# Kernel tuning notes

Measured on AMD Instinct MI355X. Metric: run time of the kernel, lower is better.

Reference implementation:

```python
import jax, jax.numpy as jnp
import numpy as np

B, C, H, W = 32, 3, 512, 512
DOWNSAMPLE = 2
N = W // DOWNSAMPLE  # 256 glimpse points
SMALL = 1e-4


def setup_inputs() -> dict:
    key = jax.random.key(0)
    k1, k2 = jax.random.split(key)
    x = jax.random.normal(k1, (B, C, H, W), dtype=jnp.float32)
    # p = locnet output: (gx_raw, gy_raw, log_sigma2, log_delta, log_gamma)
    p = jax.random.normal(k2, (B, 5), dtype=jnp.float32) * 0.5
    return {"x": x, "p": p}


def _filterbank(g, sigma2, delta, size):
    # g, sigma2, delta: [B]; returns [B, N, size]
    i = jnp.arange(N, dtype=jnp.float32)
    a = jnp.arange(size, dtype=jnp.float32)
    mu = g[:, None] + delta[:, None] * (i - N / 2.0 - 0.5)          # [B, N]
    F = jnp.exp(-((a - mu[:, :, None]) ** 2) / 2.0 / sigma2[:, None, None])  # [B, N, size]
    return F / (F.sum(axis=-1, keepdims=True) + SMALL)


def reference(x, p):
    # attention params (matches _get_attention_params)
    gx = W * (p[:, 0] + 1.0) / 2.0
    gy = H * (p[:, 1] + 1.0) / 2.0
    sigma2 = jnp.exp(p[:, 2])
    delta = jnp.exp(p[:, 3]) * (max(W, H) - 1) / (N - 1.0)
    gamma = jnp.exp(p[:, 4])
    # Gaussian filterbanks
    Fx = _filterbank(gx, sigma2, delta, W)  # [B, N, W]
    Fy = _filterbank(gy, sigma2, delta, H)  # [B, N, H]
    # read: gamma * Fy @ x @ Fx^T, expressed as two batched GEMMs
    Fyx = jnp.einsum('bnh,bchw->bcnw', Fy, x)       # [B, C, N, W]
    out = jnp.einsum('bcnw,bmw->bcnm', Fyx, Fx)     # [B, C, N, N]
    return gamma[:, None, None, None] * out
```

## Files before the change

kernel.cpp:

```cpp
#include <hip/hip_runtime.h>
#include <hip/hip_bf16.h>
#include <math.h>


namespace {

typedef __attribute__((ext_vector_type(8))) short v8s;
typedef __attribute__((ext_vector_type(4))) short v4s;
typedef __attribute__((ext_vector_type(4))) float f32x4;

constexpr int Bn = 32;
constexpr int Cc = 3;
constexpr int HW = 512;
constexpr int Nn = 256;
constexpr float SMALLF = 1e-4f;

__device__ inline unsigned short f2bf(float f) {
    __hip_bfloat16 h = __float2bfloat16(f);
    union { __hip_bfloat16 h; unsigned short u; } c;
    c.h = h;
    return c.u;
}

__device__ inline int xcd_swz(int bid, int nwg) {
    return (bid & 7) * (nwg >> 3) + (bid >> 3);
}

__device__ inline bool tile_window_g(float g, float delta, float sigma,
                                     int r0, int Trows, int& klo, int& khi) {
    float lo = g + delta * ((float)r0 - 128.5f) - 4.5f * sigma - 2.0f;
    float hi = g + delta * ((float)(r0 + Trows - 1) - 128.5f) + 4.5f * sigma + 2.0f;
    if (hi < 0.0f || lo > 511.0f) return false;
    klo = max(0, (int)floorf(lo * (1.0f / 64.0f)));
    khi = min(7, (int)floorf(hi * (1.0f / 64.0f)));
    return khi >= klo;
}

__global__ __launch_bounds__(256) void fb_kernel(const float* __restrict__ p,
                                                 unsigned short* __restrict__ Fx,
                                                 unsigned short* __restrict__ Fy) {
    const int wid  = threadIdx.x >> 6;
    const int lane = threadIdx.x & 63;
    const int rid  = blockIdx.x * 4 + wid;
    const int which = rid >> 13;
    const int r = rid & 8191;
    const int b = r >> 8;
    const int n = r & 255;

    const float* pb = p + b * 5;
    const float sigma2 = expf(pb[2]);
    const float delta  = expf(pb[3]) * (511.0f / 255.0f);
    const float g = (which == 0) ? (HW * (pb[0] + 1.0f) * 0.5f)
                                 : (HW * (pb[1] + 1.0f) * 0.5f);
    const float mu = g + delta * ((float)n - 128.5f);
    const float inv2s = 0.5f / sigma2;

    float f[8];
    float sum = 0.0f;
#pragma unroll
    for (int q = 0; q < 8; ++q) {
        float a = (float)(q * 64 + lane);
        float d = a - mu;
        f[q] = expf(-d * d * inv2s);
        sum += f[q];
    }
#pragma unroll
    for (int s = 1; s < 64; s <<= 1) sum += __shfl_xor(sum, s, 64);
    const float inv = 1.0f / (sum + SMALLF);

    unsigned short* dst = ((which == 0) ? Fx : Fy) + ((size_t)(b * Nn + n)) * HW;
#pragma unroll
    for (int q = 0; q < 8; ++q) dst[q * 64 + lane] = f2bf(f[q] * inv);
}

__device__ inline v8s frag_read(const unsigned short* __restrict__ lds, int row, int kk, int lk) {
    int byte = row * 128 + (((kk * 64) + lk * 16) ^ ((row & 7) << 4));
    return *(const v8s*)((const char*)lds + byte);
}

__global__ __launch_bounds__(256) void gemm1_kernel(const float* __restrict__ x,
                                                    const unsigned short* __restrict__ Fx_b,
                                                    const float* __restrict__ p,
                                                    unsigned short* __restrict__ G) {
    __shared__ unsigned short lds_all[2 * 64 * 64];
    unsigned short* As = lds_all;
    unsigned short* Bs = lds_all + 64 * 64;
    const int t = threadIdx.x;
    const int wg = xcd_swz(blockIdx.x, 3072);
    const int bc = wg >> 5, b = bc / 3;
    const int rem = wg & 31;
    const int h0 = (rem >> 2) * 64;
    const int m0 = (rem & 3) * 64;

    const float* pb = p + b * 5;
    const float sigma = sqrtf(expf(pb[2]));
    const float delta = expf(pb[3]) * (511.0f / 255.0f);

    {
        const float gy = HW * (pb[1] + 1.0f) * 0.5f;
        int ulo, uhi;
        if (!tile_window_g(gy, delta, sigma, 0, 256, ulo, uhi)) return;
        int ht = h0 >> 6;
        if (ht < ulo || ht > uhi) return;
    }

    const float* Ag = x + (size_t)bc * HW * HW + (size_t)h0 * HW;
    const unsigned short* Bg = Fx_b + (size_t)b * Nn * HW + (size_t)m0 * HW;

    const float gx = HW * (pb[0] + 1.0f) * 0.5f;
    int klo = 0, khi = -1;
    bool live = tile_window_g(gx, delta, sigma, m0, 64, klo, khi);

    const int wid = t >> 6, lane = t & 63, lr = lane & 15, lk = lane >> 4;
    const int wr = (wid >> 1) * 32;
    const int wc = (wid & 1) * 32;

    const int srow = t >> 2;
    const int scq  = (t & 3) * 16;

    f32x4 acc[2][2];
#pragma unroll
    for (int i = 0; i < 2; ++i)
#pragma unroll
        for (int j = 0; j < 2; ++j) acc[i][j] = (f32x4){0.f, 0.f, 0.f, 0.f};

    float4 xa[4];
    v8s    fxv[2];

#define G1_LOAD(K0)                                                              \
    {                                                                            \
        const float* s_ = Ag + (size_t)srow * HW + (K0) + scq;                   \
        xa[0] = *(const float4*)s_;                                              \
        xa[1] = *(const float4*)(s_ + 4);                                        \
        xa[2] = *(const float4*)(s_ + 8);                                        \
        xa[3] = *(const float4*)(s_ + 12);                                       \
        const unsigned short* b_ = Bg + (size_t)srow * HW + (K0) + scq;          \
        fxv[0] = *(const v8s*)b_;                                                \
        fxv[1] = *(const v8s*)(b_ + 8);                                          \
    }

    if (live) {
        G1_LOAD(klo * 64);
#pragma unroll 1
        for (int ks = klo; ks <= khi; ++ks) {
            __syncthreads();
            {
                unsigned short q[16];
#pragma unroll
                for (int i = 0; i < 4; ++i) {
                    q[i * 4 + 0] = f2bf(xa[i].x);
                    q[i * 4 + 1] = f2bf(xa[i].y);
                    q[i * 4 + 2] = f2bf(xa[i].z);
                    q[i * 4 + 3] = f2bf(xa[i].w);
                }
                int base = srow * 128;
                int sw = (srow & 7) << 4;
                *(v8s*)((char*)As + base + ((scq * 2) ^ sw))      = *(const v8s*)q;
                *(v8s*)((char*)As + base + ((scq * 2 + 16) ^ sw)) = *(const v8s*)(q + 8);
                *(v8s*)((char*)Bs + base + ((scq * 2) ^ sw))      = fxv[0];
                *(v8s*)((char*)Bs + base + ((scq * 2 + 16) ^ sw)) = fxv[1];
            }
            __syncthreads();
            if (ks < khi) G1_LOAD((ks + 1) * 64);
#pragma unroll
            for (int kk = 0; kk < 2; ++kk) {
                v8s af[2], bf[2];
#pragma unroll
                for (int mi = 0; mi < 2; ++mi) af[mi] = frag_read(As, wr + mi * 16 + lr, kk, lk);
#pragma unroll
                for (int ni = 0; ni < 2; ++ni) bf[ni] = frag_read(Bs, wc + ni * 16 + lr, kk, lk);
#pragma unroll
                for (int mi = 0; mi < 2; ++mi)
#pragma unroll
                    for (int ni = 0; ni < 2; ++ni)
                        acc[mi][ni] = __builtin_amdgcn_mfma_f32_16x16x32_bf16(af[mi], bf[ni], acc[mi][ni], 0, 0, 0);
            }
        }
    }
#undef G1_LOAD

    __syncthreads();
    {
        unsigned short* Ls = lds_all;
#pragma unroll
        for (int mi = 0; mi < 2; ++mi)
#pragma unroll
            for (int ni = 0; ni < 2; ++ni) {
                int ml = wc + ni * 16 + lr;
                int hl = wr + mi * 16 + lk * 4;
                unsigned short q[4] = {f2bf(acc[mi][ni][0]), f2bf(acc[mi][ni][1]),
                                       f2bf(acc[mi][ni][2]), f2bf(acc[mi][ni][3])};
                *(v4s*)(Ls + ml * 72 + hl) = *(const v4s*)q;
            }
        __syncthreads();
        int ml = t >> 2;
        int hc = (t & 3) * 16;
        v8s v0 = *(const v8s*)(Ls + ml * 72 + hc);
        v8s v1 = *(const v8s*)(Ls + ml * 72 + hc + 8);
        unsigned short* dst = G + (size_t)bc * Nn * HW + (size_t)(m0 + ml) * HW + h0 + hc;
        *(v8s*)dst = v0;
        *(v8s*)(dst + 8) = v1;
    }
}

__global__ __launch_bounds__(256) void gemm2_kernel(const unsigned short* __restrict__ Fy_b,
                                                    const unsigned short* __restrict__ G,
                                                    const float* __restrict__ p,
                                                    float* __restrict__ out) {
    __shared__ unsigned short As[64 * 64];
    __shared__ unsigned short Bs[64 * 64];
    const int t = threadIdx.x;
    const int wg = xcd_swz(blockIdx.x, 1536);
    const int bc = wg >> 4, b = bc / 3;
    const int rem = wg & 15;
    const int n0 = (rem >> 2) * 64;
    const int m0 = (rem & 3) * 64;

    const unsigned short* Ag = Fy_b + (size_t)b * Nn * HW + (size_t)n0 * HW;
    const unsigned short* Bg = G + (size_t)bc * Nn * HW + (size_t)m0 * HW;

    const float* pb = p + b * 5;
    const float gamma = expf(pb[4]);
    const float sigma = sqrtf(expf(pb[2]));
    const float delta = expf(pb[3]) * (511.0f / 255.0f);
    const float gy = HW * (pb[1] + 1.0f) * 0.5f;
    int klo = 0, khi = -1;
    bool live = tile_window_g(gy, delta, sigma, n0, 64, klo, khi);

    const int wid = t >> 6, lane = t & 63, lr = lane & 15, lk = lane >> 4;
    const int wr = (wid >> 1) * 32, wc = (wid & 1) * 32;

    const int srow = t >> 2;
    const int scq  = (t & 3) * 16;

    f32x4 acc[2][2];
#pragma unroll
    for (int i = 0; i < 2; ++i)
#pragma unroll
        for (int j = 0; j < 2; ++j) acc[i][j] = (f32x4){0.f, 0.f, 0.f, 0.f};

    v8s va[2], vb[2];

#define G2_LOAD(K0)                                                              \
    {                                                                            \
        const unsigned short* a_ = Ag + (size_t)srow * HW + (K0) + scq;          \
        const unsigned short* b_ = Bg + (size_t)srow * HW + (K0) + scq;          \
        va[0] = *(const v8s*)a_;                                                 \
        va[1] = *(const v8s*)(a_ + 8);                                           \
        vb[0] = *(const v8s*)b_;                                                 \
        vb[1] = *(const v8s*)(b_ + 8);                                           \
    }

    if (live) {
        G2_LOAD(klo * 64);
#pragma unroll 1
        for (int ks = klo; ks <= khi; ++ks) {
            __syncthreads();
            {
                int base = srow * 128;
                int sw = (srow & 7) << 4;
                *(v8s*)((char*)As + base + ((scq * 2) ^ sw))      = va[0];
                *(v8s*)((char*)As + base + ((scq * 2 + 16) ^ sw)) = va[1];
                *(v8s*)((char*)Bs + base + ((scq * 2) ^ sw))      = vb[0];
                *(v8s*)((char*)Bs + base + ((scq * 2 + 16) ^ sw)) = vb[1];
            }
            __syncthreads();
            if (ks < khi) G2_LOAD((ks + 1) * 64);
#pragma unroll
            for (int kk = 0; kk < 2; ++kk) {
                v8s af[2], bf[2];
#pragma unroll
                for (int mi = 0; mi < 2; ++mi) af[mi] = frag_read(As, wr + mi * 16 + lr, kk, lk);
#pragma unroll
                for (int ni = 0; ni < 2; ++ni) bf[ni] = frag_read(Bs, wc + ni * 16 + lr, kk, lk);
#pragma unroll
                for (int mi = 0; mi < 2; ++mi)
#pragma unroll
                    for (int ni = 0; ni < 2; ++ni)
                        acc[mi][ni] = __builtin_amdgcn_mfma_f32_16x16x32_bf16(af[mi], bf[ni], acc[mi][ni], 0, 0, 0);
            }
        }
    }
#undef G2_LOAD

    float* Cg = out + (size_t)bc * Nn * Nn + (size_t)n0 * Nn + m0;
#pragma unroll
    for (int mi = 0; mi < 2; ++mi)
#pragma unroll
        for (int r = 0; r < 4; ++r) {
            int row = wr + mi * 16 + lk * 4 + r;
#pragma unroll
            for (int ni = 0; ni < 2; ++ni)
                Cg[(size_t)row * Nn + wc + ni * 16 + lr] = gamma * acc[mi][ni][r];
        }
}

}

extern "C" void kernel_launch(void* const* d_in, const int* in_sizes, int n_in,
                              void* d_out, int out_size, void* d_ws, size_t ws_size,
                              hipStream_t stream) {
    const float* x = (const float*)d_in[0];
    const float* p = (const float*)d_in[1];
    float* out = (float*)d_out;

    char* ws = (char*)d_ws;
    unsigned short* Fx_b = (unsigned short*)ws;
    unsigned short* Fy_b = Fx_b + (size_t)Bn * Nn * HW;
    unsigned short* G    = Fy_b + (size_t)Bn * Nn * HW;

    hipLaunchKernelGGL(fb_kernel, dim3(4096), dim3(256), 0, stream, p, Fx_b, Fy_b);
    hipLaunchKernelGGL(gemm1_kernel, dim3(3072), dim3(256), 0, stream, x, Fx_b, p, G);
    hipLaunchKernelGGL(gemm2_kernel, dim3(1536), dim3(256), 0, stream, Fy_b, G, p, out);
}
```

Before: 44.53 us.

## Compute all four output column tiles per block in gemm1 to reuse x loads

Each gemm1 workgroup now covers a full 64-row strip of h and loops over all four 64-wide m tiles, so one x tile is loaded, converted to bf16 and written to LDS once and then reused across up to four Fx tiles, each with its own accumulators. The grid shrinks from 3072 to 768 blocks, and k-steps outside a tile's Gaussian window are skipped per tile. This cuts redundant global reads and bf16 conversion of x. In exchange it raises LDS use to 40KB and accumulator registers fourfold, and the smaller grid lowers parallelism.

```diff
diff --git a/kernel.cpp b/kernel.cpp
--- a/kernel.cpp
+++ b/kernel.cpp
@@ -82,15 +82,12 @@
                                                     const unsigned short* __restrict__ Fx_b,
                                                     const float* __restrict__ p,
                                                     unsigned short* __restrict__ G) {
-    __shared__ unsigned short lds_all[2 * 64 * 64];
+    __shared__ unsigned short lds_all[5 * 64 * 64];
     unsigned short* As = lds_all;
-    unsigned short* Bs = lds_all + 64 * 64;
     const int t = threadIdx.x;
-    const int wg = xcd_swz(blockIdx.x, 3072);
-    const int bc = wg >> 5, b = bc / 3;
-    const int rem = wg & 31;
-    const int h0 = (rem >> 2) * 64;
-    const int m0 = (rem & 3) * 64;
+    const int wg = xcd_swz(blockIdx.x, 768);
+    const int bc = wg >> 3, b = bc / 3;
+    const int h0 = (wg & 7) * 64;
 
     const float* pb = p + b * 5;
     const float sigma = sqrtf(expf(pb[2]));
@@ -105,11 +102,19 @@
     }
 
     const float* Ag = x + (size_t)bc * HW * HW + (size_t)h0 * HW;
-    const unsigned short* Bg = Fx_b + (size_t)b * Nn * HW + (size_t)m0 * HW;
-
     const float gx = HW * (pb[0] + 1.0f) * 0.5f;
-    int klo = 0, khi = -1;
-    bool live = tile_window_g(gx, delta, sigma, m0, 64, klo, khi);
+
+    int klo[4], khi[4];
+    int uklo = 8, ukhi = -1;
+#pragma unroll
+    for (int j = 0; j < 4; ++j) {
+        if (tile_window_g(gx, delta, sigma, j * 64, 64, klo[j], khi[j])) {
+            uklo = min(uklo, klo[j]);
+            ukhi = max(ukhi, khi[j]);
+        } else {
+            klo[j] = 9; khi[j] = -9;
+        }
+    }
 
     const int wid = t >> 6, lane = t & 63, lr = lane & 15, lk = lane >> 4;
     const int wr = (wid >> 1) * 32;
@@ -118,33 +123,44 @@
     const int srow = t >> 2;
     const int scq  = (t & 3) * 16;
 
-    f32x4 acc[2][2];
-#pragma unroll
-    for (int i = 0; i < 2; ++i)
-#pragma unroll
-        for (int j = 0; j < 2; ++j) acc[i][j] = (f32x4){0.f, 0.f, 0.f, 0.f};
+    f32x4 acc[4][2][2];
+#pragma unroll
+    for (int j = 0; j < 4; ++j)
+#pragma unroll
+        for (int i = 0; i < 2; ++i)
+#pragma unroll
+            for (int q = 0; q < 2; ++q) acc[j][i][q] = (f32x4){0.f, 0.f, 0.f, 0.f};
 
     float4 xa[4];
-    v8s    fxv[2];
-
-#define G1_LOAD(K0)                                                              \
+    v8s    fxv[4][2];
+
+#define LOADA(K0)                                                                \
     {                                                                            \
         const float* s_ = Ag + (size_t)srow * HW + (K0) + scq;                   \
         xa[0] = *(const float4*)s_;                                              \
         xa[1] = *(const float4*)(s_ + 4);                                        \
         xa[2] = *(const float4*)(s_ + 8);                                        \
         xa[3] = *(const float4*)(s_ + 12);                                       \
-        const unsigned short* b_ = Bg + (size_t)srow * HW + (K0) + scq;          \
-        fxv[0] = *(const v8s*)b_;                                                \
-        fxv[1] = *(const v8s*)(b_ + 8);                                          \
-    }
-
-    if (live) {
-        G1_LOAD(klo * 64);
+    }
+#define LOADB(J, K0)                                                             \
+    {                                                                            \
+        const unsigned short* b_ = Fx_b + ((size_t)b * Nn + (J) * 64 + srow) * HW + (K0) + scq; \
+        fxv[J][0] = *(const v8s*)b_;                                             \
+        fxv[J][1] = *(const v8s*)(b_ + 8);                                       \
+    }
+
+    if (ukhi >= uklo) {
+        LOADA(uklo * 64);
+#pragma unroll
+        for (int j = 0; j < 4; ++j)
+            if (uklo >= klo[j] && uklo <= khi[j]) LOADB(j, uklo * 64);
+
 #pragma unroll 1
-        for (int ks = klo; ks <= khi; ++ks) {
+        for (int ks = uklo; ks <= ukhi; ++ks) {
             __syncthreads();
             {
+                int base = srow * 128;
+                int sw = (srow & 7) << 4;
                 unsigned short q[16];
 #pragma unroll
                 for (int i = 0; i < 4; ++i) {
@@ -153,43 +169,58 @@
                     q[i * 4 + 2] = f2bf(xa[i].z);
                     q[i * 4 + 3] = f2bf(xa[i].w);
                 }
-                int base = srow * 128;
-                int sw = (srow & 7) << 4;
                 *(v8s*)((char*)As + base + ((scq * 2) ^ sw))      = *(const v8s*)q;
                 *(v8s*)((char*)As + base + ((scq * 2 + 16) ^ sw)) = *(const v8s*)(q + 8);
-                *(v8s*)((char*)Bs + base + ((scq * 2) ^ sw))      = fxv[0];
-                *(v8s*)((char*)Bs + base + ((scq * 2 + 16) ^ sw)) = fxv[1];
+#pragma unroll
+                for (int j = 0; j < 4; ++j)
+                    if (ks >= klo[j] && ks <= khi[j]) {
+                        unsigned short* Bsj = lds_all + (1 + j) * 64 * 64;
+                        *(v8s*)((char*)Bsj + base + ((scq * 2) ^ sw))      = fxv[j][0];
+                        *(v8s*)((char*)Bsj + base + ((scq * 2 + 16) ^ sw)) = fxv[j][1];
+                    }
             }
             __syncthreads();
-            if (ks < khi) G1_LOAD((ks + 1) * 64);
-#pragma unroll
-            for (int kk = 0; kk < 2; ++kk) {
-                v8s af[2], bf[2];
-#pragma unroll
-                for (int mi = 0; mi < 2; ++mi) af[mi] = frag_read(As, wr + mi * 16 + lr, kk, lk);
-#pragma unroll
-                for (int ni = 0; ni < 2; ++ni) bf[ni] = frag_read(Bs, wc + ni * 16 + lr, kk, lk);
-#pragma unroll
-                for (int mi = 0; mi < 2; ++mi)
-#pragma unroll
-                    for (int ni = 0; ni < 2; ++ni)
-                        acc[mi][ni] = __builtin_amdgcn_mfma_f32_16x16x32_bf16(af[mi], bf[ni], acc[mi][ni], 0, 0, 0);
-            }
+            if (ks < ukhi) {
+                LOADA((ks + 1) * 64);
+#pragma unroll
+                for (int j = 0; j < 4; ++j)
+                    if (ks + 1 >= klo[j] && ks + 1 <= khi[j]) LOADB(j, (ks + 1) * 64);
+            }
+#pragma unroll
+            for (int j = 0; j < 4; ++j)
+                if (ks >= klo[j] && ks <= khi[j]) {
+                    const unsigned short* Bsj = lds_all + (1 + j) * 64 * 64;
+#pragma unroll
+                    for (int kk = 0; kk < 2; ++kk) {
+                        v8s af[2], bf[2];
+#pragma unroll
+                        for (int mi = 0; mi < 2; ++mi) af[mi] = frag_read(As, wr + mi * 16 + lr, kk, lk);
+#pragma unroll
+                        for (int ni = 0; ni < 2; ++ni) bf[ni] = frag_read(Bsj, wc + ni * 16 + lr, kk, lk);
+#pragma unroll
+                        for (int mi = 0; mi < 2; ++mi)
+#pragma unroll
+                            for (int ni = 0; ni < 2; ++ni)
+                                acc[j][mi][ni] = __builtin_amdgcn_mfma_f32_16x16x32_bf16(af[mi], bf[ni], acc[j][mi][ni], 0, 0, 0);
+                    }
+                }
         }
     }
-#undef G1_LOAD
-
-    __syncthreads();
-    {
-        unsigned short* Ls = lds_all;
+#undef LOADA
+#undef LOADB
+
+    unsigned short* Ls = lds_all;
+#pragma unroll 1
+    for (int j = 0; j < 4; ++j) {
+        __syncthreads();
 #pragma unroll
         for (int mi = 0; mi < 2; ++mi)
 #pragma unroll
             for (int ni = 0; ni < 2; ++ni) {
                 int ml = wc + ni * 16 + lr;
                 int hl = wr + mi * 16 + lk * 4;
-                unsigned short q[4] = {f2bf(acc[mi][ni][0]), f2bf(acc[mi][ni][1]),
-                                       f2bf(acc[mi][ni][2]), f2bf(acc[mi][ni][3])};
+                unsigned short q[4] = {f2bf(acc[j][mi][ni][0]), f2bf(acc[j][mi][ni][1]),
+                                       f2bf(acc[j][mi][ni][2]), f2bf(acc[j][mi][ni][3])};
                 *(v4s*)(Ls + ml * 72 + hl) = *(const v4s*)q;
             }
         __syncthreads();
@@ -197,7 +228,7 @@
         int hc = (t & 3) * 16;
         v8s v0 = *(const v8s*)(Ls + ml * 72 + hc);
         v8s v1 = *(const v8s*)(Ls + ml * 72 + hc + 8);
-        unsigned short* dst = G + (size_t)bc * Nn * HW + (size_t)(m0 + ml) * HW + h0 + hc;
+        unsigned short* dst = G + (size_t)bc * Nn * HW + (size_t)(j * 64 + ml) * HW + h0 + hc;
         *(v8s*)dst = v0;
         *(v8s*)(dst + 8) = v1;
     }
@@ -310,6 +341,6 @@
     unsigned short* G    = Fy_b + (size_t)Bn * Nn * HW;
 
     hipLaunchKernelGGL(fb_kernel, dim3(4096), dim3(256), 0, stream, p, Fx_b, Fy_b);
-    hipLaunchKernelGGL(gemm1_kernel, dim3(3072), dim3(256), 0, stream, x, Fx_b, p, G);
+    hipLaunchKernelGGL(gemm1_kernel, dim3(768), dim3(256), 0, stream, x, Fx_b, p, G);
     hipLaunchKernelGGL(gemm2_kernel, dim3(1536), dim3(256), 0, stream, Fy_b, G, p, out);
 }
```

Measured after the change: 69.43 us. 55.9% more time.

## Double-buffer LDS tiles in both GEMMs to drop one barrier per k-step

Applied to the files above, without the earlier changes.

Both GEMM kernels now alternate between two LDS buffers per k-iteration, which removes the leading __syncthreads before each tile store. One barrier per step is meant to be saved, so the stores of the next tile can overlap with slower waves' MFMA reads of the previous one. LDS use per block doubles to 32 KB, which could lower occupancy. The epilogue of gemm1 reuses lds_all after its own barrier, so that path remains safe.

```diff
diff --git a/kernel.cpp b/kernel.cpp
--- a/kernel.cpp
+++ b/kernel.cpp
@@ -82,9 +82,7 @@
                                                     const unsigned short* __restrict__ Fx_b,
                                                     const float* __restrict__ p,
                                                     unsigned short* __restrict__ G) {
-    __shared__ unsigned short lds_all[2 * 64 * 64];
-    unsigned short* As = lds_all;
-    unsigned short* Bs = lds_all + 64 * 64;
+    __shared__ unsigned short lds_all[2 * 8192];
     const int t = threadIdx.x;
     const int wg = xcd_swz(blockIdx.x, 3072);
     const int bc = wg >> 5, b = bc / 3;
@@ -143,7 +141,8 @@
         G1_LOAD(klo * 64);
 #pragma unroll 1
         for (int ks = klo; ks <= khi; ++ks) {
-            __syncthreads();
+            unsigned short* Asb = lds_all + ((ks - klo) & 1) * 8192;
+            unsigned short* Bsb = Asb + 4096;
             {
                 unsigned short q[16];
 #pragma unroll
@@ -155,10 +154,10 @@
                 }
                 int base = srow * 128;
                 int sw = (srow & 7) << 4;
-                *(v8s*)((char*)As + base + ((scq * 2) ^ sw))      = *(const v8s*)q;
-                *(v8s*)((char*)As + base + ((scq * 2 + 16) ^ sw)) = *(const v8s*)(q + 8);
-                *(v8s*)((char*)Bs + base + ((scq * 2) ^ sw))      = fxv[0];
-                *(v8s*)((char*)Bs + base + ((scq * 2 + 16) ^ sw)) = fxv[1];
+                *(v8s*)((char*)Asb + base + ((scq * 2) ^ sw))      = *(const v8s*)q;
+                *(v8s*)((char*)Asb + base + ((scq * 2 + 16) ^ sw)) = *(const v8s*)(q + 8);
+                *(v8s*)((char*)Bsb + base + ((scq * 2) ^ sw))      = fxv[0];
+                *(v8s*)((char*)Bsb + base + ((scq * 2 + 16) ^ sw)) = fxv[1];
             }
             __syncthreads();
             if (ks < khi) G1_LOAD((ks + 1) * 64);
@@ -166,9 +165,9 @@
             for (int kk = 0; kk < 2; ++kk) {
                 v8s af[2], bf[2];
 #pragma unroll
-                for (int mi = 0; mi < 2; ++mi) af[mi] = frag_read(As, wr + mi * 16 + lr, kk, lk);
-#pragma unroll
-                for (int ni = 0; ni < 2; ++ni) bf[ni] = frag_read(Bs, wc + ni * 16 + lr, kk, lk);
+                for (int mi = 0; mi < 2; ++mi) af[mi] = frag_read(Asb, wr + mi * 16 + lr, kk, lk);
+#pragma unroll
+                for (int ni = 0; ni < 2; ++ni) bf[ni] = frag_read(Bsb, wc + ni * 16 + lr, kk, lk);
 #pragma unroll
                 for (int mi = 0; mi < 2; ++mi)
 #pragma unroll
@@ -207,8 +206,7 @@
                                                     const unsigned short* __restrict__ G,
                                                     const float* __restrict__ p,
                                                     float* __restrict__ out) {
-    __shared__ unsigned short As[64 * 64];
-    __shared__ unsigned short Bs[64 * 64];
+    __shared__ unsigned short lds2[2 * 8192];
     const int t = threadIdx.x;
     const int wg = xcd_swz(blockIdx.x, 1536);
     const int bc = wg >> 4, b = bc / 3;
@@ -255,14 +253,15 @@
         G2_LOAD(klo * 64);
 #pragma unroll 1
         for (int ks = klo; ks <= khi; ++ks) {
-            __syncthreads();
+            unsigned short* Asb = lds2 + ((ks - klo) & 1) * 8192;
+            unsigned short* Bsb = Asb + 4096;
             {
                 int base = srow * 128;
                 int sw = (srow & 7) << 4;
-                *(v8s*)((char*)As + base + ((scq * 2) ^ sw))      = va[0];
-                *(v8s*)((char*)As + base + ((scq * 2 + 16) ^ sw)) = va[1];
-                *(v8s*)((char*)Bs + base + ((scq * 2) ^ sw))      = vb[0];
-                *(v8s*)((char*)Bs + base + ((scq * 2 + 16) ^ sw)) = vb[1];
+                *(v8s*)((char*)Asb + base + ((scq * 2) ^ sw))      = va[0];
+                *(v8s*)((char*)Asb + base + ((scq * 2 + 16) ^ sw)) = va[1];
+                *(v8s*)((char*)Bsb + base + ((scq * 2) ^ sw))      = vb[0];
+                *(v8s*)((char*)Bsb + base + ((scq * 2 + 16) ^ sw)) = vb[1];
             }
             __syncthreads();
             if (ks < khi) G2_LOAD((ks + 1) * 64);
@@ -270,9 +269,9 @@
             for (int kk = 0; kk < 2; ++kk) {
                 v8s af[2], bf[2];
 #pragma unroll
-                for (int mi = 0; mi < 2; ++mi) af[mi] = frag_read(As, wr + mi * 16 + lr, kk, lk);
-#pragma unroll
-                for (int ni = 0; ni < 2; ++ni) bf[ni] = frag_read(Bs, wc + ni * 16 + lr, kk, lk);
+                for (int mi = 0; mi < 2; ++mi) af[mi] = frag_read(Asb, wr + mi * 16 + lr, kk, lk);
+#pragma unroll
+                for (int ni = 0; ni < 2; ++ni) bf[ni] = frag_read(Bsb, wc + ni * 16 + lr, kk, lk);
 #pragma unroll
                 for (int mi = 0; mi < 2; ++mi)
 #pragma unroll
```

Result: no change. 44.75 us (+0.5%).
